# Kernel tuning notes

Hardware: AMD Instinct MI355X
Metric: run time of the kernel (lower is better)

Reference implementation:

```python
import jax, jax.numpy as jnp
import numpy as np

DEGREE = 5
A = 1.0
B = 1.0
IN_F = 1024
OUT_F = 1024
BATCH = 8192


def setup_inputs() -> dict:
    key = jax.random.key(0)
    k1, k2, k3, k4 = jax.random.split(key, 4)
    x = jax.random.normal(k1, (BATCH, IN_F), dtype=jnp.float32)
    # base_weight ~ kaiming-uniform-ish scale
    bound_w = 1.0 / np.sqrt(IN_F)
    base_weight = jax.random.uniform(k2, (OUT_F, IN_F), dtype=jnp.float32,
                                     minval=-bound_w, maxval=bound_w)
    std = 1.0 / (IN_F * np.sqrt(DEGREE + 1))
    jacobi_coeffs = std * jax.random.normal(k3, (OUT_F, IN_F, DEGREE + 1), dtype=jnp.float32)
    bias = jax.random.uniform(k4, (OUT_F,), dtype=jnp.float32, minval=-bound_w, maxval=bound_w)
    return {"x": x, "base_weight": base_weight, "jacobi_coeffs": jacobi_coeffs, "bias": bias}


def _jacobi_polynomials(x):
    # x: (batch, in_features) -> (batch, in_features, DEGREE+1)
    t = jnp.tanh(x)
    polys = [jnp.ones_like(t)]
    if DEGREE >= 1:
        polys.append(0.5 * (2.0 * (A + 1.0) * t + (A - B)))
    for k in range(2, DEGREE + 1):
        # recurrence coefficients (matching torch loop where k = written index)
        alpha_n = 2.0 * k * (k + A + B) * (2 * k + A + B - 2)
        beta_n = (2 * k + A + B - 1) * (A ** 2 - B ** 2)
        gamma_n = (2 * k + A + B - 2) * (2 * k + A + B - 1) * (2 * k + A + B)
        delta_n = 2.0 * (k + A - 1) * (k + B - 1) * (2 * k + A + B)
        Acoef = (beta_n + alpha_n * t) / gamma_n
        Bcoef = delta_n / gamma_n
        polys.append(Acoef * polys[k - 1] - Bcoef * polys[k - 2])
    return jnp.stack(polys, axis=-1)


def reference(x, base_weight, jacobi_coeffs, bias):
    # base branch: SiLU then linear
    base_out = jax.nn.silu(x) @ base_weight.T  # (b, out)
    # jacobi branch
    P = _jacobi_polynomials(x)  # (b, in, deg+1)
    jac_out = jnp.einsum('bik,oik->bo', P, jacobi_coeffs)
    return base_out + jac_out + bias
```

## Files before the change

### kernel.cpp

```cpp
#include <hip/hip_runtime.h>
#include <hip/hip_bf16.h>
#include <cstdint>
#include <cstddef>

#define BATCH   8192
#define IN_F    1024
#define OUT_F   1024
#define KAUG    (6 * 1024)
#define NSTEP   64

typedef __bf16 bf16x8 __attribute__((ext_vector_type(8)));
typedef float  f32x4  __attribute__((ext_vector_type(4)));

static constexpr size_t WAUG_B    = (size_t)OUT_F * KAUG * 2;
static constexpr size_t BIAS2_OFF = WAUG_B;

constexpr float JA[4] = {64.f/120.f, 180.f/336.f, 384.f/720.f, 700.f/1320.f};
constexpr float JB[4] = {48.f/120.f, 144.f/336.f, 320.f/720.f, 600.f/1320.f};

__device__ __forceinline__ unsigned short f2bf(float f)
{
    __hip_bfloat16 h = __float2bfloat16(f);
    return *(unsigned short*)&h;
}
__device__ __forceinline__ unsigned pack2(float lo, float hi)
{
    return (unsigned)f2bf(lo) | ((unsigned)f2bf(hi) << 16);
}
__device__ __forceinline__ unsigned cvt_pk(float lo, float hi)
{
    unsigned r;
    asm("v_cvt_pk_bf16_f32 %0, %1, %2" : "=v"(r) : "v"(lo), "v"(hi));
    return r;
}

__global__ void prep_w(const float* __restrict__ W,
                       const float* __restrict__ C,
                       const float* __restrict__ bias,
                       __hip_bfloat16* __restrict__ Waug,
                       float* __restrict__ bias2)
{
    const int o = blockIdx.x;
    const int tid = threadIdx.x;
    const int i = tid * 4;

    const float4 wv = *(const float4*)(W + (size_t)o * IN_F + i);
    const float w4[4] = {wv.x, wv.y, wv.z, wv.w};

    float f[24];
    const float2* cp = (const float2*)(C + ((size_t)o * IN_F + i) * 6);
#pragma unroll
    for (int q = 0; q < 12; ++q) { const float2 v = cp[q]; f[q * 2] = v.x; f[q * 2 + 1] = v.y; }

    unsigned pk[12];
#pragma unroll
    for (int q = 0; q < 4; ++q) {
        pk[q * 3 + 0] = pack2(w4[q],        f[q * 6 + 1]);
        pk[q * 3 + 1] = pack2(f[q * 6 + 2], f[q * 6 + 3]);
        pk[q * 3 + 2] = pack2(f[q * 6 + 4], f[q * 6 + 5]);
    }
    uint4* dst = (uint4*)(Waug + (size_t)o * KAUG + (size_t)tid * 24);
    dst[0] = make_uint4(pk[0], pk[1], pk[2],  pk[3]);
    dst[1] = make_uint4(pk[4], pk[5], pk[6],  pk[7]);
    dst[2] = make_uint4(pk[8], pk[9], pk[10], pk[11]);

    float s = f[0] + f[6] + f[12] + f[18];
#pragma unroll
    for (int off = 32; off > 0; off >>= 1) s += __shfl_down(s, off, 64);
    __shared__ float red[4];
    if ((tid & 63) == 0) red[tid >> 6] = s;
    __syncthreads();
    if (tid == 0) bias2[o] = bias[o] + red[0] + red[1] + red[2] + red[3];
}

__device__ __forceinline__ void async_load16(const void* g, void* l)
{
    __builtin_amdgcn_global_load_lds(
        (const __attribute__((address_space(1))) void*)g,
        (__attribute__((address_space(3))) void*)l,
        16, 0, 0);
}

#define AS_B    24576
#define BS_B    24576
#define SMEM_B  (AS_B + 2 * BS_B)

__global__ __launch_bounds__(256, 2)
void gemm_kan(const float* __restrict__ X,
              const __hip_bfloat16* __restrict__ Waug,
              const float* __restrict__ bias2,
              float* __restrict__ out)
{
    extern __shared__ __align__(16) char smem[];

    const int tid  = threadIdx.x;
    const int lane = tid & 63;
    const int wave = tid >> 6;
    const int wm = wave & 1, wn = wave >> 1;
    const int mBase = blockIdx.x * 128;
    const int nBase = blockIdx.y * 128;

    const float* gx = X + (size_t)(mBase + (tid >> 1)) * IN_F + (tid & 1) * 8;
    char* const aw = smem + (tid >> 1) * 192 + (tid & 1) * 96;

    const __hip_bfloat16* gB[6]; int lB[6];
#pragma unroll
    for (int q = 0; q < 6; ++q) {
        const int ci = (q * 4 + wave) * 64 + lane;
        const int br = ci / 12, bc = ci - br * 12;
        gB[q] = Waug + (size_t)(nBase + br) * KAUG + bc * 8;
        lB[q] = AS_B + (q * 4 + wave) * 1024;
    }

    const int quad = lane >> 4, mr = lane & 15;
    const int aoff = (wm * 64 + mr) * 12 + quad;
    const int boff = (AS_B / 16) + (wn * 64 + mr) * 12 + quad;

    f32x4 acc[4][4] = {};

    float4 xc0 = *(const float4*)(gx);
    float4 xc1 = *(const float4*)(gx + 4);
#pragma unroll
    for (int q = 0; q < 6; ++q) async_load16(gB[q], smem + lB[q]);

#pragma unroll 1
    for (int t = 0; t < NSTEP; ++t) {
        const float xs[8] = {xc0.x, xc0.y, xc0.z, xc0.w, xc1.x, xc1.y, xc1.z, xc1.w};
        unsigned pk[24];
#pragma unroll
        for (int e = 0; e < 8; ++e) {
            const float x  = xs[e];
            const float v  = __expf(fminf(-x, 43.f));
            const float sg = __builtin_amdgcn_rcpf(1.f + v);
            const float s  = x * sg;
            const float u  = v * v;
            const float tt = (1.f - u) * __builtin_amdgcn_rcpf(1.f + u);
            const float p1 = 2.f * tt;
            const float p2 = JA[0] * tt * p1 - JB[0];
            const float p3 = JA[1] * tt * p2 - JB[1] * p1;
            const float p4 = JA[2] * tt * p3 - JB[2] * p2;
            const float p5 = JA[3] * tt * p4 - JB[3] * p3;
            pk[e * 3 + 0] = cvt_pk(s,  p1);
            pk[e * 3 + 1] = cvt_pk(p2, p3);
            pk[e * 3 + 2] = cvt_pk(p4, p5);
        }
        __syncthreads();
#pragma unroll
        for (int j = 0; j < 6; ++j)
            *(uint4*)(aw + j * 16) = make_uint4(pk[j * 4], pk[j * 4 + 1],
                                                pk[j * 4 + 2], pk[j * 4 + 3]);
        __syncthreads();

        if (t + 1 < NSTEP) {
            char* const bs = smem + ((t + 1) & 1) * BS_B;
#pragma unroll
            for (int q = 0; q < 6; ++q) async_load16(gB[q] + (t + 1) * 96, bs + lB[q]);
            xc0 = *(const float4*)(gx + (t + 1) * 16);
            xc1 = *(const float4*)(gx + (t + 1) * 16 + 4);
        }

        const bf16x8* V = (const bf16x8*)smem;
        const int bo = boff + (t & 1) * (BS_B / 16);
#pragma unroll
        for (int kc = 0; kc < 3; ++kc) {
            bf16x8 a[4], b[4];
#pragma unroll
            for (int t4 = 0; t4 < 4; ++t4) a[t4] = V[aoff + t4 * 192 + kc * 4];
#pragma unroll
            for (int t4 = 0; t4 < 4; ++t4) b[t4] = V[bo + t4 * 192 + kc * 4];
#pragma unroll
            for (int i = 0; i < 4; ++i)
#pragma unroll
                for (int jj = 0; jj < 4; ++jj)
                    acc[i][jj] = __builtin_amdgcn_mfma_f32_16x16x32_bf16(a[i], b[jj], acc[i][jj], 0, 0, 0);
        }
    }

#pragma unroll
    for (int i = 0; i < 4; ++i) {
#pragma unroll
        for (int jj = 0; jj < 4; ++jj) {
            const int col = nBase + wn * 64 + jj * 16 + mr;
            const float b2 = bias2[col];
#pragma unroll
            for (int r = 0; r < 4; ++r) {
                const int row = mBase + wm * 64 + i * 16 + quad * 4 + r;
                out[(size_t)row * OUT_F + col] = acc[i][jj][r] + b2;
            }
        }
    }
}


extern "C" void kernel_launch(void* const* d_in, const int* in_sizes, int n_in,
                              void* d_out, int out_size, void* d_ws, size_t ws_size,
                              hipStream_t stream)
{
    (void)out_size; (void)ws_size;
    const float* x    = (const float*)d_in[0];
    const float* W    = (const float*)d_in[1];
    const float* C    = (const float*)d_in[2];
    const float* bias = (const float*)d_in[3];
    for (int i = 0; i < n_in; ++i) {
        if      (in_sizes[i] == BATCH * IN_F)     x    = (const float*)d_in[i];
        else if (in_sizes[i] == OUT_F * IN_F)     W    = (const float*)d_in[i];
        else if (in_sizes[i] == OUT_F * IN_F * 6) C    = (const float*)d_in[i];
        else if (in_sizes[i] == OUT_F)            bias = (const float*)d_in[i];
    }
    float* out = (float*)d_out;
    char* ws = (char*)d_ws;
    __hip_bfloat16* Waug  = (__hip_bfloat16*)ws;
    float*          bias2 = (float*)(ws + BIAS2_OFF);

    static bool smem_attr_done = false;
    if (!smem_attr_done) {
        (void)hipFuncSetAttribute((const void*)gemm_kan,
                                  hipFuncAttributeMaxDynamicSharedMemorySize,
                                  SMEM_B);
        smem_attr_done = true;
    }

    prep_w<<<dim3(OUT_F), dim3(256), 0, stream>>>(W, C, bias, Waug, bias2);
    gemm_kan<<<dim3(BATCH / 128, OUT_F / 128), dim3(256), SMEM_B, stream>>>(
        x, Waug, bias2, out);
}
```

Before: 222.8 us.

## Split GEMM block into producer and MFMA consumer waves with multi-buffering

Doubles the block to 512 threads: four waves only run MFMAs from LDS while four producer waves load weights asynchronously and compute the SiLU/Jacobi expansion into double-buffered A and triple-buffered B tiles. This aims to hide the transcendental expansion and global load latency behind matrix math and halves the barriers consumers wait on. The larger LDS footprint likely limits residency to one block per CU, and consumer priority is raised with s_setprio.

Measured after the change: 236.2 us. +6.0%, slower.

```diff
diff --git a/kernel.cpp b/kernel.cpp
--- a/kernel.cpp
+++ b/kernel.cpp
@@ -83,9 +83,36 @@
 
 #define AS_B    24576
 #define BS_B    24576
-#define SMEM_B  (AS_B + 2 * BS_B)
-
-__global__ __launch_bounds__(256, 2)
+#define SMEM_B  (2 * AS_B + 3 * BS_B)
+
+__device__ __forceinline__ void expand8(const float4 x0, const float4 x1, char* dst)
+{
+    const float xs[8] = {x0.x, x0.y, x0.z, x0.w, x1.x, x1.y, x1.z, x1.w};
+    unsigned pk[24];
+#pragma unroll
+    for (int e = 0; e < 8; ++e) {
+        const float x  = xs[e];
+        const float v  = __expf(fminf(-x, 43.f));
+        const float sg = __builtin_amdgcn_rcpf(1.f + v);
+        const float s  = x * sg;
+        const float u  = v * v;
+        const float tt = (1.f - u) * __builtin_amdgcn_rcpf(1.f + u);
+        const float p1 = 2.f * tt;
+        const float p2 = JA[0] * tt * p1 - JB[0];
+        const float p3 = JA[1] * tt * p2 - JB[1] * p1;
+        const float p4 = JA[2] * tt * p3 - JB[2] * p2;
+        const float p5 = JA[3] * tt * p4 - JB[3] * p3;
+        pk[e * 3 + 0] = cvt_pk(s,  p1);
+        pk[e * 3 + 1] = cvt_pk(p2, p3);
+        pk[e * 3 + 2] = cvt_pk(p4, p5);
+    }
+#pragma unroll
+    for (int j = 0; j < 6; ++j)
+        *(uint4*)(dst + j * 16) = make_uint4(pk[j * 4], pk[j * 4 + 1],
+                                             pk[j * 4 + 2], pk[j * 4 + 3]);
+}
+
+__global__ __launch_bounds__(512, 2)
 void gemm_kan(const float* __restrict__ X,
               const __hip_bfloat16* __restrict__ Waug,
               const float* __restrict__ bias2,
@@ -96,97 +123,102 @@
     const int tid  = threadIdx.x;
     const int lane = tid & 63;
     const int wave = tid >> 6;
-    const int wm = wave & 1, wn = wave >> 1;
     const int mBase = blockIdx.x * 128;
     const int nBase = blockIdx.y * 128;
 
-    const float* gx = X + (size_t)(mBase + (tid >> 1)) * IN_F + (tid & 1) * 8;
-    char* const aw = smem + (tid >> 1) * 192 + (tid & 1) * 96;
-
-    const __hip_bfloat16* gB[6]; int lB[6];
-#pragma unroll
-    for (int q = 0; q < 6; ++q) {
-        const int ci = (q * 4 + wave) * 64 + lane;
-        const int br = ci / 12, bc = ci - br * 12;
-        gB[q] = Waug + (size_t)(nBase + br) * KAUG + bc * 8;
-        lB[q] = AS_B + (q * 4 + wave) * 1024;
-    }
-
-    const int quad = lane >> 4, mr = lane & 15;
-    const int aoff = (wm * 64 + mr) * 12 + quad;
-    const int boff = (AS_B / 16) + (wn * 64 + mr) * 12 + quad;
-
-    f32x4 acc[4][4] = {};
-
-    float4 xc0 = *(const float4*)(gx);
-    float4 xc1 = *(const float4*)(gx + 4);
-#pragma unroll
-    for (int q = 0; q < 6; ++q) async_load16(gB[q], smem + lB[q]);
-
+    if (wave < 4) {
+        const int wm = wave & 1, wn = wave >> 1;
+        const int quad = lane >> 4, mr = lane & 15;
+        const int aoff = (wm * 64 + mr) * 12 + quad;
+        const int boff = (wn * 64 + mr) * 12 + quad;
+        const int BS0  = 2 * (AS_B / 16);
+
+        f32x4 acc[4][4] = {};
+        asm volatile("s_barrier" ::: "memory");
+
+        int ab = 0, bb = 0;
+        const bf16x8* V = (const bf16x8*)smem;
 #pragma unroll 1
-    for (int t = 0; t < NSTEP; ++t) {
-        const float xs[8] = {xc0.x, xc0.y, xc0.z, xc0.w, xc1.x, xc1.y, xc1.z, xc1.w};
-        unsigned pk[24];
-#pragma unroll
-        for (int e = 0; e < 8; ++e) {
-            const float x  = xs[e];
-            const float v  = __expf(fminf(-x, 43.f));
-            const float sg = __builtin_amdgcn_rcpf(1.f + v);
-            const float s  = x * sg;
-            const float u  = v * v;
-            const float tt = (1.f - u) * __builtin_amdgcn_rcpf(1.f + u);
-            const float p1 = 2.f * tt;
-            const float p2 = JA[0] * tt * p1 - JB[0];
-            const float p3 = JA[1] * tt * p2 - JB[1] * p1;
-            const float p4 = JA[2] * tt * p3 - JB[2] * p2;
-            const float p5 = JA[3] * tt * p4 - JB[3] * p3;
-            pk[e * 3 + 0] = cvt_pk(s,  p1);
-            pk[e * 3 + 1] = cvt_pk(p2, p3);
-            pk[e * 3 + 2] = cvt_pk(p4, p5);
-        }
-        __syncthreads();
-#pragma unroll
-        for (int j = 0; j < 6; ++j)
-            *(uint4*)(aw + j * 16) = make_uint4(pk[j * 4], pk[j * 4 + 1],
-                                                pk[j * 4 + 2], pk[j * 4 + 3]);
-        __syncthreads();
-
-        if (t + 1 < NSTEP) {
-            char* const bs = smem + ((t + 1) & 1) * BS_B;
-#pragma unroll
-            for (int q = 0; q < 6; ++q) async_load16(gB[q] + (t + 1) * 96, bs + lB[q]);
-            xc0 = *(const float4*)(gx + (t + 1) * 16);
-            xc1 = *(const float4*)(gx + (t + 1) * 16 + 4);
-        }
-
-        const bf16x8* V = (const bf16x8*)smem;
-        const int bo = boff + (t & 1) * (BS_B / 16);
-#pragma unroll
-        for (int kc = 0; kc < 3; ++kc) {
-            bf16x8 a[4], b[4];
-#pragma unroll
-            for (int t4 = 0; t4 < 4; ++t4) a[t4] = V[aoff + t4 * 192 + kc * 4];
-#pragma unroll
-            for (int t4 = 0; t4 < 4; ++t4) b[t4] = V[bo + t4 * 192 + kc * 4];
-#pragma unroll
-            for (int i = 0; i < 4; ++i)
-#pragma unroll
-                for (int jj = 0; jj < 4; ++jj)
-                    acc[i][jj] = __builtin_amdgcn_mfma_f32_16x16x32_bf16(a[i], b[jj], acc[i][jj], 0, 0, 0);
-        }
-    }
-
-#pragma unroll
-    for (int i = 0; i < 4; ++i) {
-#pragma unroll
-        for (int jj = 0; jj < 4; ++jj) {
-            const int col = nBase + wn * 64 + jj * 16 + mr;
-            const float b2 = bias2[col];
-#pragma unroll
-            for (int r = 0; r < 4; ++r) {
-                const int row = mBase + wm * 64 + i * 16 + quad * 4 + r;
-                out[(size_t)row * OUT_F + col] = acc[i][jj][r] + b2;
-            }
+        for (int t = 0; t < NSTEP; ++t) {
+            const int abase = ab * (AS_B / 16) + aoff;
+            const int bbase = BS0 + bb * (BS_B / 16) + boff;
+            __builtin_amdgcn_s_setprio(1);
+#pragma unroll
+            for (int kc = 0; kc < 3; ++kc) {
+                bf16x8 a[4], b[4];
+#pragma unroll
+                for (int t4 = 0; t4 < 4; ++t4) a[t4] = V[abase + t4 * 192 + kc * 4];
+#pragma unroll
+                for (int t4 = 0; t4 < 4; ++t4) b[t4] = V[bbase + t4 * 192 + kc * 4];
+#pragma unroll
+                for (int i = 0; i < 4; ++i)
+#pragma unroll
+                    for (int jj = 0; jj < 4; ++jj)
+                        acc[i][jj] = __builtin_amdgcn_mfma_f32_16x16x32_bf16(
+                            a[i], b[jj], acc[i][jj], 0, 0, 0);
+            }
+            __builtin_amdgcn_s_setprio(0);
+            asm volatile("s_barrier" ::: "memory");
+            ab ^= 1; bb = (bb == 2) ? 0 : bb + 1;
+        }
+
+#pragma unroll
+        for (int i = 0; i < 4; ++i) {
+#pragma unroll
+            for (int jj = 0; jj < 4; ++jj) {
+                const int col = nBase + wn * 64 + jj * 16 + mr;
+                const float b2 = bias2[col];
+#pragma unroll
+                for (int r = 0; r < 4; ++r) {
+                    const int row = mBase + wm * 64 + i * 16 + quad * 4 + r;
+                    out[(size_t)row * OUT_F + col] = acc[i][jj][r] + b2;
+                }
+            }
+        }
+    } else {
+        const int ptid = tid - 256;
+        const int pw   = wave - 4;
+        const float* gx = X + (size_t)(mBase + (ptid >> 1)) * IN_F + (ptid & 1) * 8;
+        char* const awp = smem + (ptid >> 1) * 192 + (ptid & 1) * 96;
+
+        const __hip_bfloat16* gB[6]; int lB[6];
+#pragma unroll
+        for (int q = 0; q < 6; ++q) {
+            const int ci = (q * 4 + pw) * 64 + lane;
+            const int br = ci / 12, bc = ci - br * 12;
+            gB[q] = Waug + (size_t)(nBase + br) * KAUG + bc * 8;
+            lB[q] = 2 * AS_B + (q * 4 + pw) * 1024;
+        }
+
+        float4 xc0 = *(const float4*)(gx);
+        float4 xc1 = *(const float4*)(gx + 4);
+#pragma unroll
+        for (int q = 0; q < 6; ++q) async_load16(gB[q], smem + lB[q]);
+        float4 xn0 = *(const float4*)(gx + 16);
+        float4 xn1 = *(const float4*)(gx + 20);
+#pragma unroll
+        for (int q = 0; q < 6; ++q) async_load16(gB[q] + 96, smem + lB[q] + BS_B);
+        expand8(xc0, xc1, awp);
+        asm volatile("s_waitcnt vmcnt(0) lgkmcnt(0)" ::: "memory");
+        asm volatile("s_barrier" ::: "memory");
+
+        int b3 = 2;
+#pragma unroll 1
+        for (int t = 0; t < NSTEP; ++t) {
+            xc0 = xn0; xc1 = xn1;
+            if (t + 2 < NSTEP) {
+                xn0 = *(const float4*)(gx + (size_t)(t + 2) * 16);
+                xn1 = *(const float4*)(gx + (size_t)(t + 2) * 16 + 4);
+#pragma unroll
+                for (int q = 0; q < 6; ++q)
+                    async_load16(gB[q] + (size_t)(t + 2) * 96, smem + lB[q] + b3 * BS_B);
+                b3 = (b3 == 2) ? 0 : b3 + 1;
+            }
+            if (t + 1 < NSTEP) {
+                expand8(xc0, xc1, awp + ((t + 1) & 1) * AS_B);
+            }
+            asm volatile("s_waitcnt vmcnt(0) lgkmcnt(0)" ::: "memory");
+            asm volatile("s_barrier" ::: "memory");
         }
     }
 }
@@ -221,6 +253,6 @@
     }
 
     prep_w<<<dim3(OUT_F), dim3(256), 0, stream>>>(W, C, bias, Waug, bias2);
-    gemm_kan<<<dim3(BATCH / 128, OUT_F / 128), dim3(256), SMEM_B, stream>>>(
+    gemm_kan<<<dim3(BATCH / 128, OUT_F / 128), dim3(512), SMEM_B, stream>>>(
         x, Waug, bias2, out);
 }
```
